# Performance work log

Hardware: AMD Instinct MI355X
Metric: run time of the kernel (lower is better)

Reference implementation:

```python
import jax, jax.numpy as jnp
import numpy as np

N, L, H, E = 2, 2048, 8, 64
S = 2048
C_CLUSTERS = 256
ITERATIONS = 10
BITS = 32
TOPK = 32


def setup_inputs() -> dict:
    key = jax.random.key(0)
    k1, k2, k3, k4 = jax.random.split(key, 4)
    return {
        "queries": jax.random.normal(k1, (N, L, H, E), dtype=jnp.float32),
        "keys": jax.random.normal(k2, (N, S, H, E), dtype=jnp.float32),
        "values": jax.random.normal(k3, (N, S, H, E), dtype=jnp.float32),
        "planes": jax.random.normal(k4, (BITS, E + 1), dtype=jnp.float32),
    }


def _hash_bits(Q, planes):
    # Q: [N,H,L,E]; planes: [B, E+1] (last column is the hash bias)
    proj = jnp.einsum('nhle,be->nhlb', Q, planes[:, :-1]) + planes[:, -1]
    return (proj > 0).astype(jnp.float32)  # [N,H,L,B]


def _kmeans_hamming(hbits, n_clusters, iterations):
    # Lloyd iterations with hamming distance on the hash bit-vectors.
    n, h, l, b = hbits.shape
    init_idx = (jnp.arange(n_clusters) * l) // n_clusters
    cent = hbits[:, :, init_idx, :]  # [N,H,C,B], bits in {0,1}
    hsum = hbits.sum(-1)  # [N,H,L]

    def assign(cent):
        csum = cent.sum(-1)  # [N,H,C]
        # hamming(h,c) = sum_b h + sum_b c - 2 h.c for binary vectors
        dist = hsum[..., None] + csum[:, :, None, :] \
            - 2.0 * jnp.einsum('nhlb,nhcb->nhlc', hbits, cent)
        return jnp.argmin(dist, axis=-1)  # [N,H,L]

    def body(cent, _):
        a = assign(cent)
        oh = jax.nn.one_hot(a, n_clusters, dtype=jnp.float32)  # [N,H,L,C]
        counts = oh.sum(2)  # [N,H,C]
        sums = jnp.einsum('nhlc,nhlb->nhcb', oh, hbits)
        new = (sums / jnp.maximum(counts, 1.0)[..., None] >= 0.5).astype(jnp.float32)
        cent = jnp.where(counts[..., None] > 0, new, cent)  # keep empty centroids
        return cent, None

    cent, _ = jax.lax.scan(body, cent, None, length=iterations)
    a = assign(cent)
    oh = jax.nn.one_hot(a, n_clusters, dtype=jnp.float32)
    counts = oh.sum(2)
    return a, counts, oh


def reference(queries, keys, values, planes):
    Q = jnp.transpose(queries, (0, 2, 1, 3))  # [N,H,L,E]
    K = jnp.transpose(keys, (0, 2, 1, 3))     # [N,H,S,E]
    V = jnp.transpose(values, (0, 2, 1, 3))   # [N,H,S,E]
    n, h, l, e = Q.shape
    t = 1.0 / jnp.sqrt(jnp.asarray(e, jnp.float32))

    # --- hash & cluster queries (non-differentiable routing) ---
    hbits = _hash_bits(jax.lax.stop_gradient(Q), planes)
    clusters, counts, oh = _kmeans_hamming(hbits, C_CLUSTERS, ITERATIONS)

    # --- group queries: per-cluster mean (=_GroupQueries) ---
    safe = jnp.maximum(counts, 1.0)
    Qg = jnp.einsum('nhlc,nhle->nhce', oh, Q) / safe[..., None]  # [N,H,C,E]

    QK = jnp.einsum('nhce,nhse->nhcs', Qg, K)  # [N,H,C,S]; key mask is all zeros
    topv, topi = jax.lax.top_k(QK, TOPK)       # [N,H,C,k]

    # --- bottom-k attention (full softmax with top-k zeroed) ---
    A = jax.nn.softmax(t * QK, axis=-1)
    n_i = jnp.arange(n)[:, None, None, None]
    h_i = jnp.arange(h)[None, :, None, None]
    c_i = jnp.arange(C_CLUSTERS)[None, None, :, None]
    A_masked = A.at[n_i, h_i, c_i, topi].set(0.0)
    A_bk = A_masked.sum(-1)  # [N,H,C]
    Vg = jnp.einsum('nhcs,nhse->nhce', A_masked, V)  # [N,H,C,E]
    V_bottom = jnp.take_along_axis(Vg, clusters[..., None], axis=2)  # broadcast -> [N,H,L,E]
    A_bk_q = jnp.take_along_axis(A_bk, clusters, axis=2)  # [N,H,L]

    # --- top-k attention recomputed per query with its cluster's top-k keys ---
    top_q = jnp.take_along_axis(topi, clusters[..., None], axis=2)  # [N,H,L,k]
    idx = top_q.reshape(n, h, l * TOPK)[..., None]
    Kq = jnp.take_along_axis(K, idx, axis=2).reshape(n, h, l, TOPK, e)
    QKt = jnp.einsum('nhle,nhlke->nhlk', Q, Kq)
    At = jax.nn.softmax(t * QKt, axis=-1) * (1.0 - A_bk_q)[..., None]
    Vq = jnp.take_along_axis(V, idx, axis=2).reshape(n, h, l, TOPK, e)
    V_top = jnp.einsum('nhlk,nhlke->nhle', At, Vq)

    out = V_top + V_bottom  # [N,H,L,E]
    return jnp.transpose(out, (0, 2, 1, 3))  # [N,L,H,E]
```

## Files before the change

kernel.cpp:

```cpp
#include <hip/hip_runtime.h>
#include <math.h>
#include <float.h>

#define NB 2
#define LQ 2048
#define HH 8
#define EE 64
#define SS 2048
#define CC 256
#define KM_ITERS 10
#define NBITS 32
#define TK 32
#define NH (NB*HH)
#define CG 4

__global__ __launch_bounds__(256) void k_hash(const float* __restrict__ Q,
                                              const float* __restrict__ planes,
                                              unsigned int* __restrict__ qmask) {
    int gid = blockIdx.x * 256 + threadIdx.x;
    int nh = gid >> 11, l = gid & (LQ - 1);
    int n = nh >> 3, h = nh & 7;
    const float* qrow = Q + (((size_t)n * LQ + l) * HH + h) * EE;
    float q[64];
    #pragma unroll
    for (int e = 0; e < 64; e++) q[e] = qrow[e];
    unsigned int m = 0;
    for (int b = 0; b < NBITS; b++) {
        double acc = (double)planes[b * 65 + 64];
        #pragma unroll
        for (int e = 0; e < 64; e++) acc += (double)q[e] * (double)planes[b * 65 + e];
        if (acc > 0.0) m |= (1u << b);
    }
    qmask[gid] = m;
}

__global__ __launch_bounds__(256) void k_cinit(const unsigned int* __restrict__ qmask,
                                               unsigned int* __restrict__ cent_g) {
    int nh = blockIdx.x, t = threadIdx.x;
    cent_g[nh * CC + t] = qmask[(size_t)nh * LQ + t * 8];
}

__global__ __launch_bounds__(256) void k_assign(const unsigned int* __restrict__ qmask,
                                                const unsigned int* __restrict__ cent_g,
                                                int* __restrict__ asg) {
    int nh = blockIdx.x >> 3;
    int p = ((blockIdx.x & 7) << 8) + threadIdx.x;
    int t = threadIdx.x;
    __shared__ __align__(16) unsigned int cent[CC];
    cent[t] = cent_g[nh * CC + t];
    __syncthreads();
    unsigned int m = qmask[(size_t)nh * LQ + p];
    int best = 0x7fffffff;
    const uint4* c4p = (const uint4*)cent;
    #pragma unroll 4
    for (int c4 = 0; c4 < CC / 4; c4++) {
        uint4 cm = c4p[c4];
        int base = c4 << 2;
        int e0 = (__popc(m ^ cm.x) << 8) + base;
        int e1 = (__popc(m ^ cm.y) << 8) + base + 1;
        int e2 = (__popc(m ^ cm.z) << 8) + base + 2;
        int e3 = (__popc(m ^ cm.w) << 8) + base + 3;
        int e01 = e0 < e1 ? e0 : e1;
        int e23 = e2 < e3 ? e2 : e3;
        int e = e01 < e23 ? e01 : e23;
        best = best < e ? best : e;
    }
    asg[(size_t)nh * LQ + p] = best & 255;
}

__global__ __launch_bounds__(512) void k_update(const unsigned int* __restrict__ qmask,
                                                const int* __restrict__ asg,
                                                unsigned int* __restrict__ cent_g) {
    int nh = blockIdx.x, t = threadIdx.x;
    __shared__ unsigned int sorted[LQ];
    __shared__ int cnts[CC], offs[CC], cursor[CC];
    if (t < CC) cnts[t] = 0;
    int bc[4]; unsigned int mym[4];
    #pragma unroll
    for (int k = 0; k < 4; k++) {
        bc[k] = asg[(size_t)nh * LQ + t + k * 512];
        mym[k] = qmask[(size_t)nh * LQ + t + k * 512];
    }
    __syncthreads();
    #pragma unroll
    for (int k = 0; k < 4; k++) atomicAdd(&cnts[bc[k]], 1);
    __syncthreads();
    if (t < 64) {
        int c0 = cnts[4 * t], c1 = cnts[4 * t + 1], c2 = cnts[4 * t + 2], c3 = cnts[4 * t + 3];
        int s1 = c0 + c1, s2 = s1 + c2, tot = s2 + c3;
        int inc = tot;
        #pragma unroll
        for (int o = 1; o < 64; o <<= 1) {
            int v = __shfl_up(inc, o);
            if (t >= o) inc += v;
        }
        int excl = inc - tot;
        offs[4 * t] = excl;          cursor[4 * t] = excl;
        offs[4 * t + 1] = excl + c0; cursor[4 * t + 1] = excl + c0;
        offs[4 * t + 2] = excl + s1; cursor[4 * t + 2] = excl + s1;
        offs[4 * t + 3] = excl + s2; cursor[4 * t + 3] = excl + s2;
    }
    __syncthreads();
    int cl = t >> 1, j = t & 1;
    int cnt_c = cnts[cl], off_c = offs[cl];
    #pragma unroll
    for (int k = 0; k < 4; k++) {
        int pos = atomicAdd(&cursor[bc[k]], 1);
        sorted[pos] = mym[k];
    }
    __syncthreads();
    int bs[32];
    #pragma unroll
    for (int b = 0; b < 32; b++) bs[b] = 0;
    for (int i = j; i < cnt_c; i += 2) {
        unsigned int m = sorted[off_c + i];
        #pragma unroll
        for (int b = 0; b < 32; b++) bs[b] += (m >> b) & 1;
    }
    #pragma unroll
    for (int b = 0; b < 32; b++) bs[b] += __shfl_xor(bs[b], 1);
    if (j == 0 && cnt_c > 0) {
        unsigned int nc = 0;
        #pragma unroll
        for (int b = 0; b < 32; b++) if (2 * bs[b] >= cnt_c) nc |= (1u << b);
        cent_g[nh * CC + cl] = nc;
    }
}

__global__ __launch_bounds__(512) void k_finalize(const int* __restrict__ asg,
                                                  int* __restrict__ counts_out,
                                                  int* __restrict__ order_out,
                                                  int* __restrict__ offsets_out) {
    int nh = blockIdx.x, t = threadIdx.x;
    __shared__ int cnts[CC], offs[CC], cursor[CC];
    if (t < CC) cnts[t] = 0;
    int bc[4];
    #pragma unroll
    for (int k = 0; k < 4; k++) bc[k] = asg[(size_t)nh * LQ + t + k * 512];
    __syncthreads();
    #pragma unroll
    for (int k = 0; k < 4; k++) atomicAdd(&cnts[bc[k]], 1);
    __syncthreads();
    if (t < 64) {
        int c0 = cnts[4 * t], c1 = cnts[4 * t + 1], c2 = cnts[4 * t + 2], c3 = cnts[4 * t + 3];
        int s1 = c0 + c1, s2 = s1 + c2, tot = s2 + c3;
        int inc = tot;
        #pragma unroll
        for (int o = 1; o < 64; o <<= 1) {
            int v = __shfl_up(inc, o);
            if (t >= o) inc += v;
        }
        int excl = inc - tot;
        offs[4 * t] = excl;          cursor[4 * t] = excl;
        offs[4 * t + 1] = excl + c0; cursor[4 * t + 1] = excl + c0;
        offs[4 * t + 2] = excl + s1; cursor[4 * t + 2] = excl + s1;
        offs[4 * t + 3] = excl + s2; cursor[4 * t + 3] = excl + s2;
    }
    __syncthreads();
    if (t < CC) {
        counts_out[nh * CC + t] = cnts[t];
        offsets_out[nh * CC + t] = offs[t];
    }
    #pragma unroll
    for (int k = 0; k < 4; k++) {
        int pos = atomicAdd(&cursor[bc[k]], 1);
        order_out[(size_t)nh * LQ + pos] = t + k * 512;
    }
}

__global__ __launch_bounds__(256) void k_qg(const float* __restrict__ Q,
                                            const int* __restrict__ order,
                                            const int* __restrict__ offsets,
                                            const int* __restrict__ counts,
                                            double* __restrict__ Qg) {
    int nh = blockIdx.x >> 6;
    int c = (blockIdx.x & 63) * 4 + (threadIdx.x >> 6);
    int e = threadIdx.x & 63;
    int n = nh >> 3, h = nh & 7;
    int off = offsets[nh * CC + c];
    int cnt = counts[nh * CC + c];
    const int* ord = order + (size_t)nh * LQ + off;
    double acc = 0.0;
    for (int i = 0; i < cnt; i++) {
        int p = ord[i];
        acc += (double)Q[(((size_t)n * LQ + p) * HH + h) * EE + e];
    }
    double safe = cnt > 0 ? (double)cnt : 1.0;
    Qg[((size_t)(nh * CC + c)) * EE + e] = acc / safe;
}

__global__ __launch_bounds__(256) void k_transpose(const float* __restrict__ Kp,
                                                   float* __restrict__ Kt) {
    int nh = blockIdx.x >> 5;
    int s0 = (blockIdx.x & 31) * 64;
    int n = nh >> 3, h = nh & 7;
    __shared__ float tile[64][65];
    int t = threadIdx.x;
    int e = t & 63, r0 = t >> 6;
    #pragma unroll
    for (int j = 0; j < 16; j++) {
        int r = r0 * 16 + j;
        tile[r][e] = Kp[(((size_t)n * SS + s0 + r) * HH + h) * EE + e];
    }
    __syncthreads();
    int sl = t & 63, eg = t >> 6;
    #pragma unroll
    for (int j = 0; j < 16; j++) {
        int ee_ = eg * 16 + j;
        Kt[((size_t)nh * EE + ee_) * SS + s0 + sl] = tile[sl][ee_];
    }
}

__global__ __launch_bounds__(256) void k_rows(const float* __restrict__ Kt,
                                              const float* __restrict__ Vp,
                                              const double* __restrict__ Qg,
                                              int* __restrict__ topi,
                                              float* __restrict__ abk,
                                              float* __restrict__ Vg) {
    int bid = blockIdx.x;
    int nh = bid >> 6, cg = bid & 63;
    int c0 = cg * CG;
    int n = nh >> 3, h = nh & 7;
    int t = threadIdx.x, w = t >> 6, l = t & 63;

    __shared__ double xrow[CG][SS];
    __shared__ double qgl[EE][CG];
    float* wpack = (float*)&xrow[0][0];
    float* redv  = (float*)&xrow[2][0];

    qgl[t >> 2][t & 3] = Qg[((size_t)(nh * CC + c0 + (t & 3))) * EE + (t >> 2)];
    __syncthreads();

    double acc[8][CG];
    #pragma unroll
    for (int r = 0; r < 8; r++)
        #pragma unroll
        for (int c = 0; c < CG; c++) acc[r][c] = 0.0;
    const float* ktb = Kt + ((size_t)nh * EE) * SS + t;
    for (int e = 0; e < EE; e++) {
        double q0 = qgl[e][0], q1 = qgl[e][1], q2 = qgl[e][2], q3 = qgl[e][3];
        const float* kr = ktb + (size_t)e * SS;
        #pragma unroll
        for (int r = 0; r < 8; r++) {
            double kv = (double)kr[r * 256];
            acc[r][0] += q0 * kv; acc[r][1] += q1 * kv;
            acc[r][2] += q2 * kv; acc[r][3] += q3 * kv;
        }
    }
    #pragma unroll
    for (int r = 0; r < 8; r++)
        #pragma unroll
        for (int c = 0; c < CG; c++) xrow[c][t + r * 256] = acc[r][c];
    __syncthreads();

    double v[32];
    #pragma unroll
    for (int k = 0; k < 32; k++) v[k] = xrow[w][l + k * 64];

    double m = v[0];
    #pragma unroll
    for (int k = 1; k < 32; k++) m = v[k] > m ? v[k] : m;
    #pragma unroll
    for (int o = 32; o > 0; o >>= 1) { double z = __shfl_xor(m, o); m = z > m ? z : m; }

    double ds = 0.0;
    #pragma unroll
    for (int k = 0; k < 32; k++) ds += (double)expf(0.125f * (float)(v[k] - m));
    #pragma unroll
    for (int o = 32; o > 0; o >>= 1) ds += __shfl_xor(ds, o);

    unsigned ext = 0;
    double lbv = -1e301; int lbi = 1 << 30;
    #pragma unroll
    for (int k = 0; k < 32; k++)
        if (v[k] > lbv) { lbv = v[k]; lbi = l + k * 64; }
    double topsum = 0.0;
    int rowid = nh * CC + c0 + w;
    for (int kk = 0; kk < TK; kk++) {
        double bv = lbv; int bi = lbi;
        #pragma unroll
        for (int o = 32; o > 0; o >>= 1) {
            double v2 = __shfl_xor(bv, o); int i2 = __shfl_xor(bi, o);
            if (v2 > bv || (v2 == bv && i2 < bi)) { bv = v2; bi = i2; }
        }
        topsum += (double)expf(0.125f * (float)(bv - m));
        if (l == 0) topi[(size_t)rowid * TK + kk] = bi;
        if ((bi & 63) == l) {
            ext |= 1u << (bi >> 6);
            lbv = -1e301; lbi = 1 << 30;
            #pragma unroll
            for (int k = 0; k < 32; k++)
                if (!((ext >> k) & 1) && v[k] > lbv) { lbv = v[k]; lbi = l + k * 64; }
        }
    }
    if (l == 0) abk[rowid] = (float)((ds - topsum) / ds);
    __syncthreads();

    float invd = (float)(1.0 / ds);
    #pragma unroll
    for (int k = 0; k < 32; k++) {
        float wk = ((ext >> k) & 1) ? 0.0f
                 : expf(0.125f * (float)(v[k] - m)) * invd;
        wpack[(l + k * 64) * CG + w] = wk;
    }
    __syncthreads();

    {
        int e = l, grp = w;
        float a0 = 0, a1 = 0, a2 = 0, a3 = 0;
        const float* vb = Vp + (((size_t)n * SS) * HH + h) * EE + e;
        const float4* wp4 = (const float4*)wpack;
        for (int s = grp * 512; s < grp * 512 + 512; s++) {
            float4 wv = wp4[s];
            float vv = vb[(size_t)s * HH * EE];
            a0 += wv.x * vv; a1 += wv.y * vv; a2 += wv.z * vv; a3 += wv.w * vv;
        }
        redv[(grp * 4 + 0) * 64 + e] = a0;
        redv[(grp * 4 + 1) * 64 + e] = a1;
        redv[(grp * 4 + 2) * 64 + e] = a2;
        redv[(grp * 4 + 3) * 64 + e] = a3;
        __syncthreads();
        int c = w;
        float s = redv[(0 * 4 + c) * 64 + e] + redv[(1 * 4 + c) * 64 + e]
                + redv[(2 * 4 + c) * 64 + e] + redv[(3 * 4 + c) * 64 + e];
        Vg[((size_t)(nh * CC + c0 + c)) * EE + e] = s;
    }
}

__global__ __launch_bounds__(256) void k_out(const float* __restrict__ Q,
                                             const float* __restrict__ Kp,
                                             const float* __restrict__ Vp,
                                             const int* __restrict__ clusters,
                                             const int* __restrict__ topi,
                                             const float* __restrict__ abk,
                                             const float* __restrict__ Vg,
                                             float* __restrict__ out) {
    int tid = threadIdx.x, wid = tid >> 6, e = tid & 63;
    int q = blockIdx.x * 4 + wid;
    int nh = q >> 11, l = q & (LQ - 1);
    int n = nh >> 3, h = nh & 7;
    int c = clusters[q];
    float scale = 1.0f - abk[nh * CC + c];
    const int* ti = topi + (size_t)(nh * CC + c) * TK;
    float qe = Q[(((size_t)n * LQ + l) * HH + h) * EE + e];
    float myv = -INFINITY;
    for (int k = 0; k < TK; k++) {
        int idx = ti[k];
        float kv = Kp[(((size_t)n * SS + idx) * HH + h) * EE + e];
        float v = qe * kv;
        #pragma unroll
        for (int o = 32; o > 0; o >>= 1) v += __shfl_xor(v, o);
        if (e == k) myv = v;
    }
    float mv = myv;
    #pragma unroll
    for (int o = 32; o > 0; o >>= 1) { float v = __shfl_xor(mv, o); mv = v > mv ? v : mv; }
    float p = (e < TK) ? expf(0.125f * (myv - mv)) : 0.0f;
    float ssum = p;
    #pragma unroll
    for (int o = 32; o > 0; o >>= 1) ssum += __shfl_xor(ssum, o);
    float at = p / ssum * scale;
    float acc = 0.0f;
    for (int k = 0; k < TK; k++) {
        float wk = __shfl(at, k, 64);
        int idx = ti[k];
        acc += wk * Vp[(((size_t)n * SS + idx) * HH + h) * EE + e];
    }
    acc += Vg[(size_t)(nh * CC + c) * EE + e];
    out[(((size_t)n * LQ + l) * HH + h) * EE + e] = acc;
}

extern "C" void kernel_launch(void* const* d_in, const int* in_sizes, int n_in,
                              void* d_out, int out_size, void* d_ws, size_t ws_size,
                              hipStream_t stream) {
    const float* Q      = (const float*)d_in[0];
    const float* K      = (const float*)d_in[1];
    const float* V      = (const float*)d_in[2];
    const float* planes = (const float*)d_in[3];
    float* out = (float*)d_out;

    char* ws = (char*)d_ws;
    unsigned int* qmask    = (unsigned int*)(ws);
    int*          clusters = (int*)(ws + (128 << 10));
    int*          counts   = (int*)(ws + (256 << 10));
    float*        abk      = (float*)(ws + (272 << 10));
    int*          topi     = (int*)(ws + (288 << 10));
    float*        Vg       = (float*)(ws + (800 << 10));
    double*       Qg       = (double*)(ws + (1824 << 10));
    float*        Kt       = (float*)(ws + (4096 << 10));
    int*          order    = (int*)(ws + (12288 << 10));
    int*          offsets  = (int*)(ws + (12416 << 10));
    unsigned int* cent_g   = (unsigned int*)(ws + (12432 << 10));

    k_transpose<<<dim3(NH * 32), dim3(256), 0, stream>>>(K, Kt);
    k_hash<<<dim3(NH * LQ / 256), dim3(256), 0, stream>>>(Q, planes, qmask);
    k_cinit<<<dim3(NH), dim3(256), 0, stream>>>(qmask, cent_g);
    for (int it = 0; it < KM_ITERS; ++it) {
        k_assign<<<dim3(NH * 8), dim3(256), 0, stream>>>(qmask, cent_g, clusters);
        k_update<<<dim3(NH), dim3(512), 0, stream>>>(qmask, clusters, cent_g);
    }
    k_assign<<<dim3(NH * 8), dim3(256), 0, stream>>>(qmask, cent_g, clusters);
    k_finalize<<<dim3(NH), dim3(512), 0, stream>>>(clusters, counts, order, offsets);
    k_qg<<<dim3(NH * 64), dim3(256), 0, stream>>>(Q, order, offsets, counts, Qg);
    k_rows<<<dim3(NH * CC / CG), dim3(256), 0, stream>>>(Kt, V, Qg, topi, abk, Vg);
    k_out<<<dim3(NH * LQ / 4), dim3(256), 0, stream>>>(Q, K, V, clusters, topi, abk, Vg, out);
}
```

Baseline: 445.0 us.

## Restructure k_rows: per-wave contiguous key ownership, transposed V, XCD block swizzle

New measurement: 759.8 us. +70.8%, slower.

```diff
diff --git a/kernel.cpp b/kernel.cpp
--- a/kernel.cpp
+++ b/kernel.cpp
@@ -189,8 +189,8 @@
     Qg[((size_t)(nh * CC + c)) * EE + e] = acc / safe;
 }
 
-__global__ __launch_bounds__(256) void k_transpose(const float* __restrict__ Kp,
-                                                   float* __restrict__ Kt) {
+__global__ __launch_bounds__(256) void k_transpose(const float* __restrict__ Xp,
+                                                   float* __restrict__ Xt) {
     int nh = blockIdx.x >> 5;
     int s0 = (blockIdx.x & 31) * 64;
     int n = nh >> 3, h = nh & 7;
@@ -200,62 +200,52 @@
     #pragma unroll
     for (int j = 0; j < 16; j++) {
         int r = r0 * 16 + j;
-        tile[r][e] = Kp[(((size_t)n * SS + s0 + r) * HH + h) * EE + e];
+        tile[r][e] = Xp[(((size_t)n * SS + s0 + r) * HH + h) * EE + e];
     }
     __syncthreads();
     int sl = t & 63, eg = t >> 6;
     #pragma unroll
     for (int j = 0; j < 16; j++) {
         int ee_ = eg * 16 + j;
-        Kt[((size_t)nh * EE + ee_) * SS + s0 + sl] = tile[sl][ee_];
-    }
-}
-
-__global__ __launch_bounds__(256) void k_rows(const float* __restrict__ Kt,
-                                              const float* __restrict__ Vp,
-                                              const double* __restrict__ Qg,
-                                              int* __restrict__ topi,
-                                              float* __restrict__ abk,
-                                              float* __restrict__ Vg) {
+        Xt[((size_t)nh * EE + ee_) * SS + s0 + sl] = tile[sl][ee_];
+    }
+}
+
+__global__ __launch_bounds__(256, 4) void k_rows(const float* __restrict__ Kt,
+                                                 const float* __restrict__ Vt,
+                                                 const double* __restrict__ Qg,
+                                                 int* __restrict__ topi,
+                                                 float* __restrict__ abk,
+                                                 float* __restrict__ Vg) {
     int bid = blockIdx.x;
-    int nh = bid >> 6, cg = bid & 63;
+    int xcd = bid & 7, idx = bid >> 3;
+    int nh = xcd * 2 + (idx >> 6);
+    int cg = idx & 63;
     int c0 = cg * CG;
-    int n = nh >> 3, h = nh & 7;
     int t = threadIdx.x, w = t >> 6, l = t & 63;
 
-    __shared__ double xrow[CG][SS];
     __shared__ double qgl[EE][CG];
-    float* wpack = (float*)&xrow[0][0];
-    float* redv  = (float*)&xrow[2][0];
+    __shared__ float pred[CG][EE][17];
 
     qgl[t >> 2][t & 3] = Qg[((size_t)(nh * CC + c0 + (t & 3))) * EE + (t >> 2)];
     __syncthreads();
 
-    double acc[8][CG];
-    #pragma unroll
-    for (int r = 0; r < 8; r++)
-        #pragma unroll
-        for (int c = 0; c < CG; c++) acc[r][c] = 0.0;
-    const float* ktb = Kt + ((size_t)nh * EE) * SS + t;
+    double v[32];
+    #pragma unroll
+    for (int k = 0; k < 32; k++) v[k] = 0.0;
+    const float* ktb = Kt + ((size_t)nh * EE) * SS + l * 32;
     for (int e = 0; e < EE; e++) {
-        double q0 = qgl[e][0], q1 = qgl[e][1], q2 = qgl[e][2], q3 = qgl[e][3];
-        const float* kr = ktb + (size_t)e * SS;
-        #pragma unroll
-        for (int r = 0; r < 8; r++) {
-            double kv = (double)kr[r * 256];
-            acc[r][0] += q0 * kv; acc[r][1] += q1 * kv;
-            acc[r][2] += q2 * kv; acc[r][3] += q3 * kv;
-        }
-    }
-    #pragma unroll
-    for (int r = 0; r < 8; r++)
-        #pragma unroll
-        for (int c = 0; c < CG; c++) xrow[c][t + r * 256] = acc[r][c];
-    __syncthreads();
-
-    double v[32];
-    #pragma unroll
-    for (int k = 0; k < 32; k++) v[k] = xrow[w][l + k * 64];
+        double qe = qgl[e][w];
+        const float4* kr = (const float4*)(ktb + (size_t)e * SS);
+        #pragma unroll
+        for (int j = 0; j < 8; j++) {
+            float4 kv = kr[j];
+            v[4 * j + 0] += qe * (double)kv.x;
+            v[4 * j + 1] += qe * (double)kv.y;
+            v[4 * j + 2] += qe * (double)kv.z;
+            v[4 * j + 3] += qe * (double)kv.w;
+        }
+    }
 
     double m = v[0];
     #pragma unroll
@@ -269,11 +259,11 @@
     #pragma unroll
     for (int o = 32; o > 0; o >>= 1) ds += __shfl_xor(ds, o);
 
-    unsigned ext = 0;
+    unsigned ext = 0u;
     double lbv = -1e301; int lbi = 1 << 30;
     #pragma unroll
     for (int k = 0; k < 32; k++)
-        if (v[k] > lbv) { lbv = v[k]; lbi = l + k * 64; }
+        if (v[k] > lbv) { lbv = v[k]; lbi = l * 32 + k; }
     double topsum = 0.0;
     int rowid = nh * CC + c0 + w;
     for (int kk = 0; kk < TK; kk++) {
@@ -285,44 +275,46 @@
         }
         topsum += (double)expf(0.125f * (float)(bv - m));
         if (l == 0) topi[(size_t)rowid * TK + kk] = bi;
-        if ((bi & 63) == l) {
-            ext |= 1u << (bi >> 6);
+        if ((bi >> 5) == l) {
+            ext |= 1u << (bi & 31);
             lbv = -1e301; lbi = 1 << 30;
             #pragma unroll
             for (int k = 0; k < 32; k++)
-                if (!((ext >> k) & 1) && v[k] > lbv) { lbv = v[k]; lbi = l + k * 64; }
+                if (!((ext >> k) & 1) && v[k] > lbv) { lbv = v[k]; lbi = l * 32 + k; }
         }
     }
     if (l == 0) abk[rowid] = (float)((ds - topsum) / ds);
-    __syncthreads();
 
     float invd = (float)(1.0 / ds);
-    #pragma unroll
-    for (int k = 0; k < 32; k++) {
-        float wk = ((ext >> k) & 1) ? 0.0f
-                 : expf(0.125f * (float)(v[k] - m)) * invd;
-        wpack[(l + k * 64) * CG + w] = wk;
-    }
-    __syncthreads();
-
+    float w32[32];
+    #pragma unroll
+    for (int k = 0; k < 32; k++)
+        w32[k] = ((ext >> k) & 1) ? 0.0f
+               : expf(0.125f * (float)(v[k] - m)) * invd;
+
+    const float* vtb = Vt + ((size_t)nh * EE) * SS + l * 32;
+    for (int e = 0; e < EE; e++) {
+        const float4* vr = (const float4*)(vtb + (size_t)e * SS);
+        float a0 = 0.f, a1 = 0.f, a2 = 0.f, a3 = 0.f;
+        #pragma unroll
+        for (int j = 0; j < 8; j += 4) {
+            float4 v0 = vr[j], v1 = vr[j + 1], v2 = vr[j + 2], v3 = vr[j + 3];
+            a0 += w32[4 * j + 0] * v0.x + w32[4 * j + 1] * v0.y + w32[4 * j + 2] * v0.z + w32[4 * j + 3] * v0.w;
+            a1 += w32[4 * j + 4] * v1.x + w32[4 * j + 5] * v1.y + w32[4 * j + 6] * v1.z + w32[4 * j + 7] * v1.w;
+            a2 += w32[4 * j + 8] * v2.x + w32[4 * j + 9] * v2.y + w32[4 * j + 10] * v2.z + w32[4 * j + 11] * v2.w;
+            a3 += w32[4 * j + 12] * v3.x + w32[4 * j + 13] * v3.y + w32[4 * j + 14] * v3.z + w32[4 * j + 15] * v3.w;
+        }
+        float acc = (a0 + a1) + (a2 + a3);
+        acc += __shfl_xor(acc, 16);
+        acc += __shfl_xor(acc, 32);
+        if (l < 16) pred[w][e][l] = acc;
+    }
+    __syncthreads();
     {
-        int e = l, grp = w;
-        float a0 = 0, a1 = 0, a2 = 0, a3 = 0;
-        const float* vb = Vp + (((size_t)n * SS) * HH + h) * EE + e;
-        const float4* wp4 = (const float4*)wpack;
-        for (int s = grp * 512; s < grp * 512 + 512; s++) {
-            float4 wv = wp4[s];
-            float vv = vb[(size_t)s * HH * EE];
-            a0 += wv.x * vv; a1 += wv.y * vv; a2 += wv.z * vv; a3 += wv.w * vv;
-        }
-        redv[(grp * 4 + 0) * 64 + e] = a0;
-        redv[(grp * 4 + 1) * 64 + e] = a1;
-        redv[(grp * 4 + 2) * 64 + e] = a2;
-        redv[(grp * 4 + 3) * 64 + e] = a3;
-        __syncthreads();
-        int c = w;
-        float s = redv[(0 * 4 + c) * 64 + e] + redv[(1 * 4 + c) * 64 + e]
-                + redv[(2 * 4 + c) * 64 + e] + redv[(3 * 4 + c) * 64 + e];
+        int c = t >> 6, e = t & 63;
+        float s = 0.f;
+        #pragma unroll
+        for (int i = 0; i < 16; i++) s += pred[c][e][i];
         Vg[((size_t)(nh * CC + c0 + c)) * EE + e] = s;
     }
 }
@@ -391,8 +383,10 @@
     int*          order    = (int*)(ws + (12288 << 10));
     int*          offsets  = (int*)(ws + (12416 << 10));
     unsigned int* cent_g   = (unsigned int*)(ws + (12432 << 10));
+    float*        Vt       = (float*)(ws + (12544 << 10));
 
     k_transpose<<<dim3(NH * 32), dim3(256), 0, stream>>>(K, Kt);
+    k_transpose<<<dim3(NH * 32), dim3(256), 0, stream>>>(V, Vt);
     k_hash<<<dim3(NH * LQ / 256), dim3(256), 0, stream>>>(Q, planes, qmask);
     k_cinit<<<dim3(NH), dim3(256), 0, stream>>>(qmask, cent_g);
     for (int it = 0; it < KM_ITERS; ++it) {
@@ -402,6 +396,6 @@
     k_assign<<<dim3(NH * 8), dim3(256), 0, stream>>>(qmask, cent_g, clusters);
     k_finalize<<<dim3(NH), dim3(512), 0, stream>>>(clusters, counts, order, offsets);
     k_qg<<<dim3(NH * 64), dim3(256), 0, stream>>>(Q, order, offsets, counts, Qg);
-    k_rows<<<dim3(NH * CC / CG), dim3(256), 0, stream>>>(Kt, V, Qg, topi, abk, Vg);
+    k_rows<<<dim3(NH * CC / CG), dim3(256), 0, stream>>>(Kt, Vt, Qg, topi, abk, Vg);
     k_out<<<dim3(NH * LQ / 4), dim3(256), 0, stream>>>(Q, K, V, clusters, topi, abk, Vg, out);
 }
```

## Chunk k_rows shared staging to shrink LDS and remap blocks per XCD

Applied to the files above, without the earlier changes.

New measurement: 421.4 us, median of 3. -5.3%, faster.

```diff
diff --git a/kernel.cpp b/kernel.cpp
--- a/kernel.cpp
+++ b/kernel.cpp
@@ -218,15 +218,17 @@
                                               float* __restrict__ abk,
                                               float* __restrict__ Vg) {
     int bid = blockIdx.x;
-    int nh = bid >> 6, cg = bid & 63;
+    int xcd = bid & 7, idx = bid >> 3;
+    int nh = xcd * 2 + (idx >> 6);
+    int cg = idx & 63;
     int c0 = cg * CG;
     int n = nh >> 3, h = nh & 7;
     int t = threadIdx.x, w = t >> 6, l = t & 63;
 
-    __shared__ double xrow[CG][SS];
     __shared__ double qgl[EE][CG];
-    float* wpack = (float*)&xrow[0][0];
-    float* redv  = (float*)&xrow[2][0];
+    __shared__ double xrowc[CG][512];
+    float* wbuf = (float*)&xrowc[0][0];
+    float* redv = (float*)&xrowc[2][0];
 
     qgl[t >> 2][t & 3] = Qg[((size_t)(nh * CC + c0 + (t & 3))) * EE + (t >> 2)];
     __syncthreads();
@@ -247,15 +249,21 @@
             acc[r][2] += q2 * kv; acc[r][3] += q3 * kv;
         }
     }
-    #pragma unroll
-    for (int r = 0; r < 8; r++)
-        #pragma unroll
-        for (int c = 0; c < CG; c++) xrow[c][t + r * 256] = acc[r][c];
-    __syncthreads();
 
     double v[32];
     #pragma unroll
-    for (int k = 0; k < 32; k++) v[k] = xrow[w][l + k * 64];
+    for (int j = 0; j < 4; j++) {
+        __syncthreads();
+        #pragma unroll
+        for (int c = 0; c < CG; c++) {
+            xrowc[c][t]       = acc[2 * j][c];
+            xrowc[c][256 + t] = acc[2 * j + 1][c];
+        }
+        __syncthreads();
+        #pragma unroll
+        for (int m = 0; m < 8; m++)
+            v[8 * j + m] = xrowc[w][((m >> 2) << 8) + ((m & 3) << 6) + l];
+    }
 
     double m = v[0];
     #pragma unroll
@@ -294,27 +302,33 @@
         }
     }
     if (l == 0) abk[rowid] = (float)((ds - topsum) / ds);
-    __syncthreads();
 
     float invd = (float)(1.0 / ds);
-    #pragma unroll
-    for (int k = 0; k < 32; k++) {
-        float wk = ((ext >> k) & 1) ? 0.0f
-                 : expf(0.125f * (float)(v[k] - m)) * invd;
-        wpack[(l + k * 64) * CG + w] = wk;
-    }
-    __syncthreads();
-
+    float w32r[32];
+    #pragma unroll
+    for (int k = 0; k < 32; k++)
+        w32r[k] = ((ext >> k) & 1) ? 0.0f
+                : expf(0.125f * (float)(v[k] - m)) * invd;
+
+    float a0 = 0.f, a1 = 0.f, a2 = 0.f, a3 = 0.f;
+    const float* vb = Vp + (((size_t)n * SS) * HH + h) * EE + l;
+    #pragma unroll
+    for (int j = 0; j < 4; j++) {
+        __syncthreads();
+        #pragma unroll
+        for (int m2 = 0; m2 < 8; m2++)
+            wbuf[(((m2 << 6) + l) << 2) + w] = w32r[8 * j + m2];
+        __syncthreads();
+        const float4* wp4 = (const float4*)wbuf;
+        int sbase = 512 * j + 128 * w;
+        for (int s = 0; s < 128; s++) {
+            float4 wv = wp4[128 * w + s];
+            float vv = vb[(size_t)(sbase + s) * HH * EE];
+            a0 += wv.x * vv; a1 += wv.y * vv; a2 += wv.z * vv; a3 += wv.w * vv;
+        }
+    }
     {
         int e = l, grp = w;
-        float a0 = 0, a1 = 0, a2 = 0, a3 = 0;
-        const float* vb = Vp + (((size_t)n * SS) * HH + h) * EE + e;
-        const float4* wp4 = (const float4*)wpack;
-        for (int s = grp * 512; s < grp * 512 + 512; s++) {
-            float4 wv = wp4[s];
-            float vv = vb[(size_t)s * HH * EE];
-            a0 += wv.x * vv; a1 += wv.y * vv; a2 += wv.z * vv; a3 += wv.w * vv;
-        }
         redv[(grp * 4 + 0) * 64 + e] = a0;
         redv[(grp * 4 + 1) * 64 + e] = a1;
         redv[(grp * 4 + 2) * 64 + e] = a2;
```
